# Kernel optimization log

Measured on AMD Instinct MI355X. Metric: run time of the kernel, lower is better.

The kernel has to match this reference:

```python
import jax, jax.numpy as jnp
import numpy as np

B, S, D, H, F, M = 2, 2048, 1024, 16, 4096, 1024
HD = D // H
LR, MOM_DECAY, WD, THRESH = 0.01, 0.9, 0.01, 0.1


def rmsnorm(x, w, eps=1e-8):
    n = jnp.linalg.norm(x, axis=-1, keepdims=True) * (x.shape[-1] ** -0.5)
    return w * x / (n + eps)


def rope_sin_cos(seq_len, dim):
    inv_freq = 1.0 / (10000.0 ** (jnp.arange(0, dim, 2, dtype=jnp.float32) / dim))
    ang = jnp.arange(seq_len, dtype=jnp.float32)[:, None] * inv_freq[None, :]  # [S, dim/2]
    return jnp.sin(ang), jnp.cos(ang)


def apply_rope(x, sin, cos):
    # x: [B,H,S,hd]; sin/cos: [S,hd/2] broadcast. Matches torch source:
    # split even/odd lanes, then CONCATENATE halves (not interleave).
    x1, x2 = x[..., ::2], x[..., 1::2]
    return jnp.concatenate([x1 * cos - x2 * sin, x1 * sin + x2 * cos], axis=-1)


def lmm_mlp(z, w0, b0, w1, b1):
    return jnp.maximum(z @ w0 + b0, 0.0) @ w1 + b1


def setup_inputs() -> dict:
    key = jax.random.key(0)
    k = jax.random.split(key, 20)
    sc = 0.02
    r = lambda i, shape: jax.random.normal(k[i], shape, jnp.float32) * sc
    return {
        'x': jax.random.normal(k[0], (B, S, D), jnp.float32),
        'mask': jnp.tril(jnp.ones((1, 1, S, S), dtype=bool)),
        'wq': r(1, (D, D)), 'wk': r(2, (D, D)), 'wv': r(3, (D, D)), 'wo': r(4, (D, D)),
        'n1': jnp.ones(D, jnp.float32), 'n2': jnp.ones(D, jnp.float32), 'n3': jnp.ones(D, jnp.float32),
        'ffn_w1': r(5, (D, F)), 'ffn_w2': r(6, (D, F)), 'ffn_w3': r(7, (F, D)),
        'pk_w': r(8, (D, M)), 'pk_b': jnp.zeros(M, jnp.float32),
        'pv_w': r(9, (D, M)), 'pv_b': jnp.zeros(M, jnp.float32),
        'pq_w': r(10, (D, M)), 'pq_b': jnp.zeros(M, jnp.float32),
        'l0_w': r(11, (M, M)), 'l0_b': jnp.zeros(M, jnp.float32),
        'l1_w': r(12, (M, M)), 'l1_b': jnp.zeros(M, jnp.float32),
        'm0_w': jnp.zeros((M, M), jnp.float32), 'm0_b': jnp.zeros(M, jnp.float32),
        'm1_w': jnp.zeros((M, M), jnp.float32), 'm1_b': jnp.zeros(M, jnp.float32),
    }


def reference(x, mask, wq, wk, wv, wo, n1, n2, n3, ffn_w1, ffn_w2, ffn_w3,
              pk_w, pk_b, pv_w, pv_b, pq_w, pq_b,
              l0_w, l0_b, l1_w, l1_b, m0_w, m0_b, m1_w, m1_b):
    # ---- attention sublayer (pre-norm, RoPE) ----
    hn = rmsnorm(x, n1)
    q = (hn @ wq).reshape(B, S, H, HD).transpose(0, 2, 1, 3)
    kk = (hn @ wk).reshape(B, S, H, HD).transpose(0, 2, 1, 3)
    v = (hn @ wv).reshape(B, S, H, HD).transpose(0, 2, 1, 3)
    sin, cos = rope_sin_cos(S, HD)
    q = apply_rope(q, sin, cos)
    kk = apply_rope(kk, sin, cos)
    scores = jnp.einsum('bhqd,bhkd->bhqk', q, kk) / np.sqrt(HD).astype(np.float32)
    scores = jnp.where(mask, scores, -jnp.inf)
    attn = jax.nn.softmax(scores, axis=-1)
    o = jnp.einsum('bhqk,bhkd->bhqd', attn, v).transpose(0, 2, 1, 3).reshape(B, S, D)
    h = x + o @ wo

    # ---- neural memory sublayer ----
    hn2 = rmsnorm(h, n2)
    q_lmm = hn2 @ pq_w + pq_b
    retrieved = lmm_mlp(q_lmm, l0_w, l0_b, l1_w, l1_b)  # uses PRE-update params

    # online Titan-style LMM update (torch does this under no_grad, after retrieval)
    kf = jax.lax.stop_gradient((hn2 @ pk_w + pk_b).reshape(B * S, M))
    vf = jax.lax.stop_gradient((hn2 @ pv_w + pv_b).reshape(B * S, M))

    def lmm_loss(params):
        pred = lmm_mlp(kf, *params)
        return jnp.sum(jnp.mean((pred - vf) ** 2, axis=-1))

    params = (l0_w, l0_b, l1_w, l1_b)
    loss_sum, grads = jax.value_and_grad(lmm_loss)(params)
    avg_loss = loss_sum / (B * S)
    do_update = avg_loss >= THRESH
    moms = (m0_w, m0_b, m1_w, m1_b)
    new_moms, new_params = [], []
    for p, m, g in zip(params, moms, grads):
        nm = MOM_DECAY * m - LR * g
        np_ = p * (1.0 - WD) + nm
        new_moms.append(jnp.where(do_update, nm, m))
        new_params.append(jnp.where(do_update, np_, p))

    h = h + retrieved

    # ---- SwiGLU FFN sublayer ----
    hn3 = rmsnorm(h, n3)
    ffn = (jax.nn.silu(hn3 @ ffn_w1) * (hn3 @ ffn_w2)) @ ffn_w3
    out = h + ffn
    return (out, *new_params, *new_moms)
```

## Files before the change

### kernel.cpp

```cpp
#include <hip/hip_runtime.h>
#include <cstdint>
#include <cstddef>

typedef __bf16 bf16;
typedef __bf16 bf16x2 __attribute__((ext_vector_type(2)));
typedef __bf16 bf16x4 __attribute__((ext_vector_type(4)));
typedef __bf16 bf16x8 __attribute__((ext_vector_type(8)));
typedef float  f32x4  __attribute__((ext_vector_type(4)));
typedef __attribute__((address_space(1))) unsigned int u32_g;
typedef __attribute__((address_space(3))) unsigned int u32_l;

#define DI __device__ __forceinline__

constexpr int Bc = 2, Sc = 2048, Dc = 1024, Hc = 16, HDc = 64, Fc = 4096, Mc = 1024;
constexpr int NTc = Bc * Sc;

DI void llds16(const bf16* g, bf16* l) {
  __builtin_amdgcn_global_load_lds((const u32_g*)g, (u32_l*)l, 16, 0, 0);
}
DI f32x4 cvt4(bf16x4 a) {
  f32x4 r; r[0] = (float)a[0]; r[1] = (float)a[1]; r[2] = (float)a[2]; r[3] = (float)a[3];
  return r;
}

__global__ void k_detect(const unsigned short* __restrict__ x, int* __restrict__ flag)
{
  const int tid = threadIdx.x;
  int cnt = 0;
#pragma unroll
  for (int i = 0; i < 8; i++) {
    unsigned short h = x[tid * 8 + i];
    int e = (h >> 7) & 0xFF;
    if (e < 96 || e > 160) cnt++;
  }
#pragma unroll
  for (int off = 32; off > 0; off >>= 1) cnt += __shfl_down(cnt, off, 64);
  if (tid == 0) *flag = (cnt > 32) ? 1 : 0;
}

__global__ __launch_bounds__(256)
void k_cvt(const void* __restrict__ src, bf16* __restrict__ dst, int n4, const int* __restrict__ flag)
{
  int i = blockIdx.x * 256 + threadIdx.x;
  if (i >= n4) return;
  bf16x4 o;
  if (*flag) {
    f32x4 v = ((const f32x4*)src)[i];
    o[0] = (bf16)v[0]; o[1] = (bf16)v[1]; o[2] = (bf16)v[2]; o[3] = (bf16)v[3];
  } else {
    o = ((const bf16x4*)src)[i];
  }
  ((bf16x4*)dst)[i] = o;
}

__global__ void k_transpose_dt(const void* __restrict__ src, bf16* __restrict__ dst,
                               int R, int C, const int* __restrict__ flag)
{
  __shared__ bf16 tile[32][33];
  const int c0 = blockIdx.x * 32, r0 = blockIdx.y * 32;
  const int tx = threadIdx.x, ty = threadIdx.y;
  const bool f32 = (*flag != 0);
  for (int i = ty; i < 32; i += 8) {
    size_t idx = (size_t)(r0 + i) * C + (c0 + tx);
    tile[i][tx] = f32 ? (bf16)((const float*)src)[idx] : ((const bf16*)src)[idx];
  }
  __syncthreads();
  for (int i = ty; i < 32; i += 8)
    dst[(size_t)(c0 + i) * R + (r0 + tx)] = tile[tx][i];
}

__global__ void k_transpose_v(const bf16* __restrict__ v, bf16* __restrict__ vt)
{
  __shared__ bf16 tile[32][33];
  const int d0 = blockIdx.x * 32, s0 = blockIdx.y * 32;
  const int bh = blockIdx.z;
  const int b = bh >> 4, hh = bh & 15;
  const int tx = threadIdx.x, ty = threadIdx.y;
  for (int i = ty; i < 32; i += 8)
    tile[i][tx] = v[((size_t)(b * Sc + s0 + i)) * Dc + hh * HDc + d0 + tx];
  __syncthreads();
  for (int i = ty; i < 32; i += 8)
    vt[((size_t)(bh * HDc + d0 + i)) * Sc + s0 + tx] = tile[tx][i];
}

enum EpiMode { EPI_BF16 = 0, EPI_BIAS_BF16, EPI_BIAS_RELU_BF16, EPI_BIAS_RESB_F32,
               EPI_SILU_BF16, EPI_DZ_BF16, EPI_RESX_BF16, EPI_RESF_F32 };

template <int EPI>
__global__ __launch_bounds__(256)
void k_gemm(const bf16* __restrict__ A, const bf16* __restrict__ Bt,
            int Mr, int Nr, int Kr,
            float* outF, bf16* outB,
            const bf16* __restrict__ bias, const bf16* auxB,
            const float* resF,
            const void* __restrict__ resX, const int* __restrict__ flag)
{
  __shared__ bf16 As[128 * 32];
  __shared__ bf16 Bs[128 * 32];
  const int tid = threadIdx.x;
  const int w = tid >> 6, l = tid & 63;
  const int wr = w >> 1, wc = w & 1;
  const int row0 = blockIdx.y * 128, col0 = blockIdx.x * 128;

  const f32x4 vzero = {0.f, 0.f, 0.f, 0.f};
  f32x4 acc[4][4];
#pragma unroll
  for (int i = 0; i < 4; i++)
#pragma unroll
    for (int j = 0; j < 4; j++) acc[i][j] = vzero;

  const bf16* Ag = A + (size_t)(row0 + w * 16 + (l >> 2)) * Kr + ((l & 3) << 3);
  const bf16* Bg = Bt + (size_t)(col0 + w * 16 + (l >> 2)) * Kr + ((l & 3) << 3);
  bf16* AsW = &As[w * 512];
  bf16* BsW = &Bs[w * 512];
  const size_t rowHop = (size_t)64 * Kr;

  for (int k0 = 0; k0 < Kr; k0 += 32) {
    __syncthreads();
    llds16(Ag + k0, AsW);
    llds16(Ag + rowHop + k0, AsW + 2048);
    llds16(Bg + k0, BsW);
    llds16(Bg + rowHop + k0, BsW + 2048);
    __syncthreads();
    bf16x8 af[4], bfr[4];
#pragma unroll
    for (int mt = 0; mt < 4; mt++)
      af[mt] = *(const bf16x8*)&As[(wr * 64 + mt * 16 + (l & 15)) * 32 + (l >> 4) * 8];
#pragma unroll
    for (int nt = 0; nt < 4; nt++)
      bfr[nt] = *(const bf16x8*)&Bs[(wc * 64 + nt * 16 + (l & 15)) * 32 + (l >> 4) * 8];
#pragma unroll
    for (int mt = 0; mt < 4; mt++)
#pragma unroll
      for (int nt = 0; nt < 4; nt++)
        acc[mt][nt] = __builtin_amdgcn_mfma_f32_16x16x32_bf16(af[mt], bfr[nt], acc[mt][nt], 0, 0, 0);
  }

  const bool f32res = (EPI == EPI_RESX_BF16) ? (*flag != 0) : false;
  float biasv[4];
  if (EPI == EPI_BIAS_BF16 || EPI == EPI_BIAS_RELU_BF16 || EPI == EPI_BIAS_RESB_F32) {
#pragma unroll
    for (int nt = 0; nt < 4; nt++)
      biasv[nt] = (float)bias[col0 + wc * 64 + nt * 16 + (l & 15)];
  }
#pragma unroll
  for (int mt = 0; mt < 4; mt++) {
    const int rowb = row0 + wr * 64 + mt * 16 + ((l >> 4) << 2);
    float av[4][4];
    if (EPI == EPI_SILU_BF16 || EPI == EPI_DZ_BF16 || EPI == EPI_BIAS_RESB_F32) {
#pragma unroll
      for (int nt = 0; nt < 4; nt++) {
        const int col = col0 + wc * 64 + nt * 16 + (l & 15);
#pragma unroll
        for (int r = 0; r < 4; r++)
          av[nt][r] = (float)auxB[(size_t)(rowb + r) * Nr + col];
      }
    }
    if (EPI == EPI_RESF_F32) {
#pragma unroll
      for (int nt = 0; nt < 4; nt++) {
        const int col = col0 + wc * 64 + nt * 16 + (l & 15);
#pragma unroll
        for (int r = 0; r < 4; r++)
          av[nt][r] = resF[(size_t)(rowb + r) * Nr + col];
      }
    }
    if (EPI == EPI_RESX_BF16) {
#pragma unroll
      for (int nt = 0; nt < 4; nt++) {
        const int col = col0 + wc * 64 + nt * 16 + (l & 15);
#pragma unroll
        for (int r = 0; r < 4; r++) {
          const size_t idx = (size_t)(rowb + r) * Nr + col;
          av[nt][r] = f32res ? ((const float*)resX)[idx] : (float)((const bf16*)resX)[idx];
        }
      }
    }
#pragma unroll
    for (int nt = 0; nt < 4; nt++) {
      const int col = col0 + wc * 64 + nt * 16 + (l & 15);
#pragma unroll
      for (int r = 0; r < 4; r++) {
        const size_t idx = (size_t)(rowb + r) * Nr + col;
        float v = acc[mt][nt][r];
        if (EPI == EPI_BF16) { outB[idx] = (bf16)v; }
        else if (EPI == EPI_BIAS_BF16) { outB[idx] = (bf16)(v + biasv[nt]); }
        else if (EPI == EPI_BIAS_RELU_BF16) { outB[idx] = (bf16)fmaxf(v + biasv[nt], 0.f); }
        else if (EPI == EPI_BIAS_RESB_F32) { outF[idx] = v + biasv[nt] + av[nt][r]; }
        else if (EPI == EPI_SILU_BF16) {
          float s1v = av[nt][r];
          float sl = s1v / (1.f + __expf(-s1v));
          outB[idx] = (bf16)(sl * v);
        }
        else if (EPI == EPI_DZ_BF16) { outB[idx] = (bf16)(av[nt][r] > 0.f ? v : 0.f); }
        else if (EPI == EPI_RESX_BF16) { outB[idx] = (bf16)(v + av[nt][r]); }
        else if (EPI == EPI_RESF_F32) { outF[idx] = v + av[nt][r]; }
      }
    }
  }
}

__global__ __launch_bounds__(256)
void k_gemm_tn(const bf16* __restrict__ X, const bf16* __restrict__ Y, int Kt,
               float* __restrict__ out)
{
  __shared__ bf16 As[128 * 36];
  __shared__ bf16 Bs[128 * 36];
  const int tid = threadIdx.x;
  const int w = tid >> 6, l = tid & 63;
  const int wr = w >> 1, wc = w & 1;
  const int row0 = blockIdx.y * 128, col0 = blockIdx.x * 128;
  const int iofs = (tid & 15) * 8;
  const int tp   = (tid >> 4) * 2;

  const f32x4 vzero = {0.f, 0.f, 0.f, 0.f};
  f32x4 acc[4][4];
#pragma unroll
  for (int i = 0; i < 4; i++)
#pragma unroll
    for (int j = 0; j < 4; j++) acc[i][j] = vzero;

  const int chunk = Kt / gridDim.z;
  const int tbeg = blockIdx.z * chunk;

  for (int t0 = tbeg; t0 < tbeg + chunk; t0 += 32) {
    __syncthreads();
    bf16x8 a0 = *(const bf16x8*)&X[(size_t)(t0 + tp) * 1024 + row0 + iofs];
    bf16x8 a1 = *(const bf16x8*)&X[(size_t)(t0 + tp + 1) * 1024 + row0 + iofs];
    bf16x8 b0 = *(const bf16x8*)&Y[(size_t)(t0 + tp) * 1024 + col0 + iofs];
    bf16x8 b1 = *(const bf16x8*)&Y[(size_t)(t0 + tp + 1) * 1024 + col0 + iofs];
#pragma unroll
    for (int e = 0; e < 8; e++) {
      bf16x2 pa; pa[0] = a0[e]; pa[1] = a1[e];
      bf16x2 pb; pb[0] = b0[e]; pb[1] = b1[e];
      *(bf16x2*)&As[(iofs + e) * 36 + tp] = pa;
      *(bf16x2*)&Bs[(iofs + e) * 36 + tp] = pb;
    }
    __syncthreads();
    bf16x8 af[4], bfr[4];
#pragma unroll
    for (int mt = 0; mt < 4; mt++) {
      const int base = (wr * 64 + mt * 16 + (l & 15)) * 36 + (l >> 4) * 8;
      bf16x4 lo = *(const bf16x4*)&As[base];
      bf16x4 hi = *(const bf16x4*)&As[base + 4];
#pragma unroll
      for (int e = 0; e < 4; e++) { af[mt][e] = lo[e]; af[mt][4 + e] = hi[e]; }
    }
#pragma unroll
    for (int nt = 0; nt < 4; nt++) {
      const int base = (wc * 64 + nt * 16 + (l & 15)) * 36 + (l >> 4) * 8;
      bf16x4 lo = *(const bf16x4*)&Bs[base];
      bf16x4 hi = *(const bf16x4*)&Bs[base + 4];
#pragma unroll
      for (int e = 0; e < 4; e++) { bfr[nt][e] = lo[e]; bfr[nt][4 + e] = hi[e]; }
    }
#pragma unroll
    for (int mt = 0; mt < 4; mt++)
#pragma unroll
      for (int nt = 0; nt < 4; nt++)
        acc[mt][nt] = __builtin_amdgcn_mfma_f32_16x16x32_bf16(af[mt], bfr[nt], acc[mt][nt], 0, 0, 0);
  }

#pragma unroll
  for (int mt = 0; mt < 4; mt++) {
    const int rowb = row0 + wr * 64 + mt * 16 + ((l >> 4) << 2);
#pragma unroll
    for (int nt = 0; nt < 4; nt++) {
      const int col = col0 + wc * 64 + nt * 16 + (l & 15);
#pragma unroll
      for (int r = 0; r < 4; r++)
        atomicAdd(&out[(size_t)(rowb + r) * 1024 + col], acc[mt][nt][r]);
    }
  }
}

__global__ __launch_bounds__(256)
void k_rmsnorm_dt(const void* __restrict__ x, const bf16* __restrict__ w, bf16* __restrict__ out,
                  const int* __restrict__ flag)
{
  const int row = blockIdx.x;
  const int tid = threadIdx.x;
  f32x4 xv;
  if (*flag) xv = *(const f32x4*)((const float*)x + (size_t)row * Dc + tid * 4);
  else       xv = cvt4(*(const bf16x4*)((const bf16*)x + (size_t)row * Dc + tid * 4));
  float ss = xv[0] * xv[0] + xv[1] * xv[1] + xv[2] * xv[2] + xv[3] * xv[3];
#pragma unroll
  for (int off = 32; off > 0; off >>= 1) ss += __shfl_down(ss, off, 64);
  __shared__ float part[4];
  if ((tid & 63) == 0) part[tid >> 6] = ss;
  __syncthreads();
  float tot = part[0] + part[1] + part[2] + part[3];
  float inv = 1.f / (sqrtf(tot) * 0.03125f + 1e-8f);
  bf16x4 wb = *(const bf16x4*)(w + tid * 4);
  bf16x4 ov;
  ov[0] = (bf16)((float)wb[0] * xv[0] * inv);
  ov[1] = (bf16)((float)wb[1] * xv[1] * inv);
  ov[2] = (bf16)((float)wb[2] * xv[2] * inv);
  ov[3] = (bf16)((float)wb[3] * xv[3] * inv);
  *(bf16x4*)(out + (size_t)row * Dc + tid * 4) = ov;
}

__global__ __launch_bounds__(256)
void k_rmsnorm_b(const bf16* __restrict__ x, const bf16* __restrict__ w, bf16* __restrict__ out)
{
  const int row = blockIdx.x;
  const int tid = threadIdx.x;
  f32x4 xv = cvt4(*(const bf16x4*)(x + (size_t)row * Dc + tid * 4));
  float ss = xv[0] * xv[0] + xv[1] * xv[1] + xv[2] * xv[2] + xv[3] * xv[3];
#pragma unroll
  for (int off = 32; off > 0; off >>= 1) ss += __shfl_down(ss, off, 64);
  __shared__ float part[4];
  if ((tid & 63) == 0) part[tid >> 6] = ss;
  __syncthreads();
  float tot = part[0] + part[1] + part[2] + part[3];
  float inv = 1.f / (sqrtf(tot) * 0.03125f + 1e-8f);
  bf16x4 wb = *(const bf16x4*)(w + tid * 4);
  bf16x4 ov;
  ov[0] = (bf16)((float)wb[0] * xv[0] * inv);
  ov[1] = (bf16)((float)wb[1] * xv[1] * inv);
  ov[2] = (bf16)((float)wb[2] * xv[2] * inv);
  ov[3] = (bf16)((float)wb[3] * xv[3] * inv);
  *(bf16x4*)(out + (size_t)row * Dc + tid * 4) = ov;
}

__global__ __launch_bounds__(256)
void k_rmsnorm_f(const float* __restrict__ x, const bf16* __restrict__ w, bf16* __restrict__ out)
{
  const int row = blockIdx.x;
  const int tid = threadIdx.x;
  f32x4 xv = *(const f32x4*)(x + (size_t)row * Dc + tid * 4);
  float ss = xv[0] * xv[0] + xv[1] * xv[1] + xv[2] * xv[2] + xv[3] * xv[3];
#pragma unroll
  for (int off = 32; off > 0; off >>= 1) ss += __shfl_down(ss, off, 64);
  __shared__ float part[4];
  if ((tid & 63) == 0) part[tid >> 6] = ss;
  __syncthreads();
  float tot = part[0] + part[1] + part[2] + part[3];
  float inv = 1.f / (sqrtf(tot) * 0.03125f + 1e-8f);
  bf16x4 wb = *(const bf16x4*)(w + tid * 4);
  bf16x4 ov;
  ov[0] = (bf16)((float)wb[0] * xv[0] * inv);
  ov[1] = (bf16)((float)wb[1] * xv[1] * inv);
  ov[2] = (bf16)((float)wb[2] * xv[2] * inv);
  ov[3] = (bf16)((float)wb[3] * xv[3] * inv);
  *(bf16x4*)(out + (size_t)row * Dc + tid * 4) = ov;
}

__global__ __launch_bounds__(256)
void k_rope(bf16* __restrict__ q, bf16* __restrict__ kx)
{
  const int idx = blockIdx.x * 256 + threadIdx.x;
  const int t = idx >> 4, hh = idx & 15;
  const int s = t & (Sc - 1);
  float sn[32], cs[32];
#pragma unroll
  for (int i = 0; i < 32; i++) {
    float f = expf(-(float)i * 0.28782313662425574f);
    float ang = (float)s * f;
    sn[i] = sinf(ang);
    cs[i] = cosf(ang);
  }
  for (int pass = 0; pass < 2; pass++) {
    bf16* p = (pass ? kx : q) + (size_t)t * Dc + hh * HDc;
    float xb[64], ob[64];
#pragma unroll
    for (int j = 0; j < 16; j++) *(f32x4*)&xb[j * 4] = cvt4(*(const bf16x4*)(p + j * 4));
#pragma unroll
    for (int i = 0; i < 32; i++) {
      float x1 = xb[2 * i], x2 = xb[2 * i + 1];
      ob[i] = x1 * cs[i] - x2 * sn[i];
      ob[32 + i] = x1 * sn[i] + x2 * cs[i];
    }
#pragma unroll
    for (int j = 0; j < 16; j++) {
      bf16x4 o4;
      o4[0] = (bf16)ob[j * 4]; o4[1] = (bf16)ob[j * 4 + 1];
      o4[2] = (bf16)ob[j * 4 + 2]; o4[3] = (bf16)ob[j * 4 + 3];
      *(bf16x4*)(p + j * 4) = o4;
    }
  }
}

__global__ __launch_bounds__(256)
void k_attn(const bf16* __restrict__ q, const bf16* __restrict__ kx,
            const bf16* __restrict__ vt, bf16* __restrict__ o)
{
  constexpr int PAD = 72;
  __shared__ __align__(16) char smem[19456];

  const int blk = blockIdx.x;
  const int qi = 127 - (blk >> 5);
  const int bh = blk & 31;
  const int b = bh >> 4, hh = bh & 15;
  const int tid = threadIdx.x;
  const int w = tid >> 6, l = tid & 63;
  const int quad = l >> 4, c = l & 15;

  bf16* Psw = (bf16*)smem + w * 16 * PAD;
  float* Buf = (float*)smem;

  const int qrow = qi * 16 + c;
  const size_t qbase = ((size_t)(b * Sc + qrow)) * Dc + hh * HDc;
  bf16x8 qf0 = *(const bf16x8*)(q + qbase + quad * 8);
  bf16x8 qf1 = *(const bf16x8*)(q + qbase + 32 + quad * 8);
#pragma unroll
  for (int j = 0; j < 8; j++) {
    qf0[j] = (bf16)((float)qf0[j] * 0.125f);
    qf1[j] = (bf16)((float)qf1[j] * 0.125f);
  }

  const f32x4 vzero = {0.f, 0.f, 0.f, 0.f};
  f32x4 oacc[4];
#pragma unroll
  for (int nt = 0; nt < 4; nt++) oacc[nt] = vzero;
  float mrun[4] = {-3.0e38f, -3.0e38f, -3.0e38f, -3.0e38f};
  float lrun[4] = {0.f, 0.f, 0.f, 0.f};

  const int qrow0 = qi * 16 + quad * 4;
  const int ntiles = (qi >> 2) + 1;

  const bf16* kb = kx + (size_t)b * Sc * Dc + hh * HDc;
  const bf16* vb = vt + (size_t)bh * HDc * Sc;

  for (int t0 = w; t0 < ntiles; t0 += 4) {
    const int kk0 = t0 * 64;

    f32x4 sf[4];
#pragma unroll
    for (int nt = 0; nt < 4; nt++) {
      const bf16* kr = kb + (size_t)(kk0 + nt * 16 + c) * Dc + quad * 8;
      bf16x8 k0 = *(const bf16x8*)kr;
      bf16x8 k1 = *(const bf16x8*)(kr + 32);
      f32x4 a = vzero;
      a = __builtin_amdgcn_mfma_f32_16x16x32_bf16(qf0, k0, a, 0, 0, 0);
      a = __builtin_amdgcn_mfma_f32_16x16x32_bf16(qf1, k1, a, 0, 0, 0);
      sf[nt] = a;
    }
    if (t0 == ntiles - 1) {
#pragma unroll
      for (int nt = 0; nt < 4; nt++)
#pragma unroll
        for (int r = 0; r < 4; r++)
          if (kk0 + nt * 16 + c > qrow0 + r) sf[nt][r] = -3.0e38f;
    }

    float mnew[4], alpha[4];
#pragma unroll
    for (int r = 0; r < 4; r++) {
      float mt = fmaxf(fmaxf(sf[0][r], sf[1][r]), fmaxf(sf[2][r], sf[3][r]));
      mt = fmaxf(mt, __shfl_xor(mt, 1, 64));
      mt = fmaxf(mt, __shfl_xor(mt, 2, 64));
      mt = fmaxf(mt, __shfl_xor(mt, 4, 64));
      mt = fmaxf(mt, __shfl_xor(mt, 8, 64));
      mnew[r] = fmaxf(mrun[r], mt);
      alpha[r] = __expf(mrun[r] - mnew[r]);
      mrun[r] = mnew[r];
    }
    float ps[4] = {0.f, 0.f, 0.f, 0.f};
#pragma unroll
    for (int nt = 0; nt < 4; nt++)
#pragma unroll
      for (int r = 0; r < 4; r++) {
        float p = __expf(sf[nt][r] - mnew[r]);
        sf[nt][r] = p;
        ps[r] += p;
      }
#pragma unroll
    for (int r = 0; r < 4; r++) {
      ps[r] += __shfl_xor(ps[r], 1, 64);
      ps[r] += __shfl_xor(ps[r], 2, 64);
      ps[r] += __shfl_xor(ps[r], 4, 64);
      ps[r] += __shfl_xor(ps[r], 8, 64);
      lrun[r] = lrun[r] * alpha[r] + ps[r];
    }
#pragma unroll
    for (int nt = 0; nt < 4; nt++)
#pragma unroll
      for (int r = 0; r < 4; r++) oacc[nt][r] *= alpha[r];

#pragma unroll
    for (int nt = 0; nt < 4; nt++)
#pragma unroll
      for (int r = 0; r < 4; r++)
        Psw[(quad * 4 + r) * PAD + nt * 16 + c] = (bf16)sf[nt][r];
    bf16x8 pa0 = *(const bf16x8*)&Psw[c * PAD + quad * 8];
    bf16x8 pa1 = *(const bf16x8*)&Psw[c * PAD + 32 + quad * 8];

#pragma unroll
    for (int nt = 0; nt < 4; nt++) {
      const bf16* vr = vb + (size_t)(nt * 16 + c) * Sc + kk0 + quad * 8;
      bf16x8 v0 = *(const bf16x8*)vr;
      bf16x8 v1 = *(const bf16x8*)(vr + 32);
      oacc[nt] = __builtin_amdgcn_mfma_f32_16x16x32_bf16(pa0, v0, oacc[nt], 0, 0, 0);
      oacc[nt] = __builtin_amdgcn_mfma_f32_16x16x32_bf16(pa1, v1, oacc[nt], 0, 0, 0);
    }
  }

  __syncthreads();
  if (w > 0) {
    float* dst = Buf + ((w - 1) * 64 + l) * 25;
#pragma unroll
    for (int nt = 0; nt < 4; nt++)
#pragma unroll
      for (int r = 0; r < 4; r++) dst[nt * 4 + r] = oacc[nt][r];
#pragma unroll
    for (int r = 0; r < 4; r++) { dst[16 + r] = mrun[r]; dst[20 + r] = lrun[r]; }
  }
  __syncthreads();
  if (w == 0) {
#pragma unroll
    for (int w2 = 0; w2 < 3; w2++) {
      const float* src = Buf + (w2 * 64 + l) * 25;
      float m2[4], l2[4];
#pragma unroll
      for (int r = 0; r < 4; r++) { m2[r] = src[16 + r]; l2[r] = src[20 + r]; }
#pragma unroll
      for (int r = 0; r < 4; r++) {
        float mn = fmaxf(mrun[r], m2[r]);
        float a = __expf(mrun[r] - mn);
        float bb = __expf(m2[r] - mn);
        lrun[r] = lrun[r] * a + l2[r] * bb;
        mrun[r] = mn;
#pragma unroll
        for (int nt = 0; nt < 4; nt++)
          oacc[nt][r] = oacc[nt][r] * a + src[nt * 4 + r] * bb;
      }
    }
    float inv[4];
#pragma unroll
    for (int r = 0; r < 4; r++) inv[r] = 1.f / lrun[r];
#pragma unroll
    for (int r = 0; r < 4; r++) {
      const size_t obase = ((size_t)(b * Sc + qrow0 + r)) * Dc + hh * HDc;
#pragma unroll
      for (int nt = 0; nt < 4; nt++)
        o[obase + nt * 16 + c] = (bf16)(oacc[nt][r] * inv[r]);
    }
  }
}

__global__ __launch_bounds__(256)
void k_relu(const bf16* __restrict__ src, bf16* __restrict__ dst)
{
  int i = blockIdx.x * 256 + threadIdx.x;
  bf16x8 v = ((const bf16x8*)src)[i];
  bf16x8 o;
#pragma unroll
  for (int e = 0; e < 8; e++) o[e] = ((float)v[e] > 0.f) ? v[e] : (bf16)0.f;
  ((bf16x8*)dst)[i] = o;
}

__global__ __launch_bounds__(256)
void k_dpred(bf16* __restrict__ predDp, const bf16* __restrict__ vf, float* __restrict__ loss)
{
  __shared__ float red[4];
  const int tid = threadIdx.x;
  const size_t n8 = (size_t)NTc * Mc / 8;
  float lacc = 0.f;
  for (size_t i = (size_t)blockIdx.x * 256 + tid; i < n8; i += (size_t)gridDim.x * 256) {
    bf16x8 p8 = ((const bf16x8*)predDp)[i];
    bf16x8 v8 = ((const bf16x8*)vf)[i];
    bf16x8 d8;
#pragma unroll
    for (int e = 0; e < 8; e++) {
      float df = (float)p8[e] - (float)v8[e];
      lacc += df * df;
      d8[e] = (bf16)(df * (2.0f / 1024.0f));
    }
    ((bf16x8*)predDp)[i] = d8;
  }
#pragma unroll
  for (int off = 32; off > 0; off >>= 1) lacc += __shfl_down(lacc, off, 64);
  if ((tid & 63) == 0) red[tid >> 6] = lacc;
  __syncthreads();
  if (tid == 0) atomicAdd(loss, red[0] + red[1] + red[2] + red[3]);
}

__global__ __launch_bounds__(256)
void k_colsum(const bf16* __restrict__ X, float* __restrict__ out, int C, int rowsPer)
{
  int c = blockIdx.x * 256 + threadIdx.x;
  int r0 = blockIdx.y * rowsPer;
  float s = 0.f;
#pragma unroll 8
  for (int r = r0; r < r0 + rowsPer; r++) s += (float)X[(size_t)r * C + c];
  atomicAdd(&out[c], s);
}

__global__ __launch_bounds__(256)
void k_update_dt(const void* __restrict__ p0w, const void* __restrict__ p0b,
                 const void* __restrict__ p1w, const void* __restrict__ p1b,
                 const void* __restrict__ m0w, const void* __restrict__ m0b,
                 const void* __restrict__ m1w, const void* __restrict__ m1b,
                 const float* __restrict__ g0wF, const float* __restrict__ g0b,
                 const float* __restrict__ g1wF, const float* __restrict__ g1b,
                 const float* __restrict__ loss, const int* __restrict__ flag,
                 float* __restrict__ outP, float* __restrict__ outM)
{
  const int i = blockIdx.x * 256 + threadIdx.x;
  const bool upd = (loss[0] >= 0.1f * 1024.f * 4096.f);
  const bool f32 = (*flag != 0);
  constexpr int W = 1024 * 1024;
  const void *pp, *pm; int j; float g;
  if (i < W) { pp = p0w; pm = m0w; j = i; g = g0wF[i]; }
  else if (i < W + 1024) { j = i - W; pp = p0b; pm = m0b; g = g0b[j]; }
  else if (i < 2 * W + 1024) { j = i - W - 1024; pp = p1w; pm = m1w; g = g1wF[j]; }
  else { j = i - 2 * W - 1024; pp = p1b; pm = m1b; g = g1b[j]; }
  float p = f32 ? ((const float*)pp)[j] : (float)((const bf16*)pp)[j];
  float m = f32 ? ((const float*)pm)[j] : (float)((const bf16*)pm)[j];
  float nm = 0.9f * m - 0.01f * g;
  float np = 0.99f * p + nm;
  outP[i] = upd ? np : p;
  outM[i] = upd ? nm : m;
}

extern "C" void kernel_launch(void* const* d_in, const int* in_sizes, int n_in,
                              void* d_out, int out_size, void* d_ws, size_t ws_size,
                              hipStream_t stream)
{
  (void)in_sizes; (void)n_in; (void)out_size; (void)ws_size;
  const void* x   = d_in[0];
  const void* wq  = d_in[2];
  const void* wk  = d_in[3];
  const void* wv  = d_in[4];
  const void* wo  = d_in[5];
  const void* n1  = d_in[6];
  const void* n2  = d_in[7];
  const void* n3  = d_in[8];
  const void* fw1 = d_in[9];
  const void* fw2 = d_in[10];
  const void* fw3 = d_in[11];
  const void* pkw = d_in[12];
  const void* pkb = d_in[13];
  const void* pvw = d_in[14];
  const void* pvb = d_in[15];
  const void* pqw = d_in[16];
  const void* pqb = d_in[17];
  const void* l0w = d_in[18];
  const void* l0b = d_in[19];
  const void* l1w = d_in[20];
  const void* l1b = d_in[21];
  const void* m0w = d_in[22];
  const void* m0b = d_in[23];
  const void* m1w = d_in[24];
  const void* m1b = d_in[25];

  char* ws = (char*)d_ws;
  size_t off = 0;
  auto alloc = [&](size_t bytes) -> char* {
    char* p = ws + off;
    off += (bytes + 255) & ~(size_t)255;
    return p;
  };

  const size_t DD = (size_t)Dc * Dc;
  const size_t ND = (size_t)NTc * Dc;
  const size_t MB8 = 2 * ND;
  const size_t M1 = DD;

  bf16* W = (bf16*)alloc(2 * 8 * M1);
  bf16 *wqT = W, *wkT = W + M1, *wvT = W + 2 * M1, *woT = W + 3 * M1;
  bf16 *pqT = W + 4 * M1, *pkT = W + 5 * M1, *pvT = W + 6 * M1, *l0T = W + 7 * M1;
  bf16 *l1T = W + M1;
  bf16 *l1c = W;
  bf16 *w1T = W + 4 * M1;
  bf16 *w2T = W;
  bf16 *w3T = W + 4 * M1;

  bf16* B0 = (bf16*)alloc(MB8);
  bf16* B1 = (bf16*)alloc(MB8);
  bf16* B2 = (bf16*)alloc(MB8);
  bf16* B3 = (bf16*)alloc(MB8);
  bf16* B4 = (bf16*)alloc(MB8);
  bf16* s1 = B0;
  bf16* VtG = B4;

  float* g0b = (float*)alloc(4 * 1024);
  float* g1b = (float*)alloc(4 * 1024);
  float* lossb = (float*)alloc(256);
  int*   flag  = (int*)alloc(256);
  bf16* n1c = (bf16*)alloc(2 * 1024);
  bf16* n2c = (bf16*)alloc(2 * 1024);
  bf16* n3c = (bf16*)alloc(2 * 1024);
  bf16* bqc = (bf16*)alloc(2 * 1024);
  bf16* bkc = (bf16*)alloc(2 * 1024);
  bf16* bvc = (bf16*)alloc(2 * 1024);
  bf16* b0c = (bf16*)alloc(2 * 1024);
  bf16* b1c = (bf16*)alloc(2 * 1024);

  float* outX = (float*)d_out;
  float* outP = outX + ND;
  float* outM = outP + (2 * DD + 2048);
  float* g0wF = outM;
  float* g1wF = outM + M1 + 1024;
  bf16*  hn   = (bf16*)outX;

  const dim3 tb(32, 8);

  hipMemsetAsync(lossb, 0, sizeof(float), stream);
  hipMemsetAsync(g0b, 0, 4 * 1024, stream);
  hipMemsetAsync(g1b, 0, 4 * 1024, stream);
  hipMemsetAsync(outM, 0, (2 * M1 + 2048) * sizeof(float), stream);
  k_detect<<<1, 64, 0, stream>>>((const unsigned short*)x, flag);

  k_cvt<<<1, 256, 0, stream>>>(n1, n1c, 256, flag);
  k_cvt<<<1, 256, 0, stream>>>(n2, n2c, 256, flag);
  k_cvt<<<1, 256, 0, stream>>>(n3, n3c, 256, flag);
  k_cvt<<<1, 256, 0, stream>>>(pqb, bqc, 256, flag);
  k_cvt<<<1, 256, 0, stream>>>(pkb, bkc, 256, flag);
  k_cvt<<<1, 256, 0, stream>>>(pvb, bvc, 256, flag);
  k_cvt<<<1, 256, 0, stream>>>(l0b, b0c, 256, flag);
  k_cvt<<<1, 256, 0, stream>>>(l1b, b1c, 256, flag);

  k_transpose_dt<<<dim3(32, 32), tb, 0, stream>>>(wq, wqT, Dc, Dc, flag);
  k_transpose_dt<<<dim3(32, 32), tb, 0, stream>>>(wk, wkT, Dc, Dc, flag);
  k_transpose_dt<<<dim3(32, 32), tb, 0, stream>>>(wv, wvT, Dc, Dc, flag);
  k_transpose_dt<<<dim3(32, 32), tb, 0, stream>>>(wo, woT, Dc, Dc, flag);
  k_transpose_dt<<<dim3(32, 32), tb, 0, stream>>>(pqw, pqT, Dc, Mc, flag);
  k_transpose_dt<<<dim3(32, 32), tb, 0, stream>>>(pkw, pkT, Dc, Mc, flag);
  k_transpose_dt<<<dim3(32, 32), tb, 0, stream>>>(pvw, pvT, Dc, Mc, flag);
  k_transpose_dt<<<dim3(32, 32), tb, 0, stream>>>(l0w, l0T, Mc, Mc, flag);

  k_rmsnorm_dt<<<NTc, 256, 0, stream>>>(x, n1c, hn, flag);
  k_gemm<EPI_BF16><<<dim3(8, 32), 256, 0, stream>>>(hn, wqT, NTc, Dc, Dc, nullptr, B0, nullptr, nullptr, nullptr, nullptr, nullptr);
  k_gemm<EPI_BF16><<<dim3(8, 32), 256, 0, stream>>>(hn, wkT, NTc, Dc, Dc, nullptr, B1, nullptr, nullptr, nullptr, nullptr, nullptr);
  k_gemm<EPI_BF16><<<dim3(8, 32), 256, 0, stream>>>(hn, wvT, NTc, Dc, Dc, nullptr, B2, nullptr, nullptr, nullptr, nullptr, nullptr);
  k_transpose_v<<<dim3(2, 64, 32), tb, 0, stream>>>(B2, VtG);
  k_rope<<<256, 256, 0, stream>>>(B0, B1);
  k_attn<<<4096, 256, 0, stream>>>(B0, B1, VtG, B3);
  k_gemm<EPI_RESX_BF16><<<dim3(8, 32), 256, 0, stream>>>(B3, woT, NTc, Dc, Dc, nullptr, B4, nullptr, nullptr, nullptr, x, flag);
  k_transpose_dt<<<dim3(32, 32), tb, 0, stream>>>(l1w, l1T, Mc, Mc, flag);

  k_rmsnorm_b<<<NTc, 256, 0, stream>>>(B4, n2c, B0);
  k_gemm<EPI_BIAS_BF16><<<dim3(8, 32), 256, 0, stream>>>(B0, pqT, NTc, Mc, Dc, nullptr, B1, bqc, nullptr, nullptr, nullptr, nullptr);
  k_gemm<EPI_BIAS_BF16><<<dim3(8, 32), 256, 0, stream>>>(B0, pkT, NTc, Mc, Dc, nullptr, B2, bkc, nullptr, nullptr, nullptr, nullptr);
  k_gemm<EPI_BIAS_BF16><<<dim3(8, 32), 256, 0, stream>>>(B0, pvT, NTc, Mc, Dc, nullptr, B3, bvc, nullptr, nullptr, nullptr, nullptr);
  k_gemm<EPI_BIAS_RELU_BF16><<<dim3(8, 32), 256, 0, stream>>>(B1, l0T, NTc, Mc, Mc, nullptr, B0, b0c, nullptr, nullptr, nullptr, nullptr);
  k_gemm<EPI_BIAS_RESB_F32><<<dim3(8, 32), 256, 0, stream>>>(B0, l1T, NTc, Mc, Mc, outX, nullptr, b1c, B4, nullptr, nullptr, nullptr);

  k_gemm<EPI_BIAS_BF16><<<dim3(8, 32), 256, 0, stream>>>(B2, l0T, NTc, Mc, Mc, nullptr, B4, b0c, nullptr, nullptr, nullptr, nullptr);
  k_transpose_dt<<<dim3(128, 32), tb, 0, stream>>>(fw1, w1T, Dc, Fc, flag);
  k_relu<<<2048, 256, 0, stream>>>(B4, B0);
  k_gemm<EPI_BIAS_BF16><<<dim3(8, 32), 256, 0, stream>>>(B0, l1T, NTc, Mc, Mc, nullptr, B1, b1c, nullptr, nullptr, nullptr, nullptr);
  k_cvt<<<1024, 256, 0, stream>>>(l1w, l1c, (int)(DD / 4), flag);
  k_dpred<<<256, 256, 0, stream>>>(B1, B3, lossb);
  k_gemm<EPI_DZ_BF16><<<dim3(8, 32), 256, 0, stream>>>(B1, l1c, NTc, Mc, Mc, nullptr, B3, nullptr, B4, nullptr, nullptr, nullptr);
  k_gemm_tn<<<dim3(8, 8, 8), 256, 0, stream>>>(B0, B1, NTc, g1wF);
  k_gemm_tn<<<dim3(8, 8, 8), 256, 0, stream>>>(B2, B3, NTc, g0wF);
  k_colsum<<<dim3(4, 32), 256, 0, stream>>>(B1, g1b, Mc, NTc / 32);
  k_colsum<<<dim3(4, 32), 256, 0, stream>>>(B3, g0b, Mc, NTc / 32);
  k_update_dt<<<8200, 256, 0, stream>>>(l0w, l0b, l1w, l1b, m0w, m0b, m1w, m1b,
                                        g0wF, g0b, g1wF, g1b, lossb, flag, outP, outM);

  k_transpose_dt<<<dim3(128, 32), tb, 0, stream>>>(fw2, w2T, Dc, Fc, flag);
  k_rmsnorm_f<<<NTc, 256, 0, stream>>>(outX, n3c, B4);
  k_gemm<EPI_BF16><<<dim3(32, 32), 256, 0, stream>>>(B4, w1T, NTc, Fc, Dc, nullptr, s1, nullptr, nullptr, nullptr, nullptr, nullptr);
  k_transpose_dt<<<dim3(32, 128), tb, 0, stream>>>(fw3, w3T, Fc, Dc, flag);
  k_gemm<EPI_SILU_BF16><<<dim3(32, 32), 256, 0, stream>>>(B4, w2T, NTc, Fc, Dc, nullptr, s1, nullptr, s1, nullptr, nullptr, nullptr);
  k_gemm<EPI_RESF_F32><<<dim3(8, 32), 256, 0, stream>>>(s1, w3T, NTc, Dc, Fc, outX, nullptr, nullptr, nullptr, outX, nullptr, nullptr);
}
```

Before: 1.091 ms.

## Batch QKV and LMM projections into wide GEMMs, split-K final FFN with atomics

The three Q/K/V projections become one N=3072 GEMM, and the three LMM pq/pk/pv projections become another, each writing into separate output segments. The two l0 forward passes (retrieval and key path) are merged into one 2*NT-row GEMM with a fused ReLU, which drops the separate relu kernel and one GEMM launch. The final FFN down-projection is split along K into two slices that accumulate into the residual output with float atomicAdd, giving more blocks for this long-K GEMM. The changes assume the projection weight transposes and the B buffers sit contiguously in memory, and the atomic accumulation makes the floating-point summation order nondeterministic.

```diff
diff --git a/kernel.cpp b/kernel.cpp
--- a/kernel.cpp
+++ b/kernel.cpp
@@ -84,7 +84,8 @@
 }
 
 enum EpiMode { EPI_BF16 = 0, EPI_BIAS_BF16, EPI_BIAS_RELU_BF16, EPI_BIAS_RESB_F32,
-               EPI_SILU_BF16, EPI_DZ_BF16, EPI_RESX_BF16, EPI_RESF_F32 };
+               EPI_SILU_BF16, EPI_DZ_BF16, EPI_RESX_BF16, EPI_RESF_F32,
+               EPI_SEGC_BF16, EPI_SEGC_BIAS_BF16, EPI_SEG2_RELU_BF16, EPI_ATOMIC_F32 };
 
 template <int EPI>
 __global__ __launch_bounds__(256)
@@ -115,7 +116,10 @@
   bf16* BsW = &Bs[w * 512];
   const size_t rowHop = (size_t)64 * Kr;
 
-  for (int k0 = 0; k0 < Kr; k0 += 32) {
+  const int chunk = Kr / gridDim.z;
+  const int kbeg = blockIdx.z * chunk;
+
+  for (int k0 = kbeg; k0 < kbeg + chunk; k0 += 32) {
     __syncthreads();
     llds16(Ag + k0, AsW);
     llds16(Ag + rowHop + k0, AsW + 2048);
@@ -138,7 +142,8 @@
 
   const bool f32res = (EPI == EPI_RESX_BF16) ? (*flag != 0) : false;
   float biasv[4];
-  if (EPI == EPI_BIAS_BF16 || EPI == EPI_BIAS_RELU_BF16 || EPI == EPI_BIAS_RESB_F32) {
+  if (EPI == EPI_BIAS_BF16 || EPI == EPI_BIAS_RELU_BF16 || EPI == EPI_BIAS_RESB_F32 ||
+      EPI == EPI_SEGC_BIAS_BF16 || EPI == EPI_SEG2_RELU_BF16) {
 #pragma unroll
     for (int nt = 0; nt < 4; nt++)
       biasv[nt] = (float)bias[col0 + wc * 64 + nt * 16 + (l & 15)];
@@ -195,6 +200,19 @@
         else if (EPI == EPI_DZ_BF16) { outB[idx] = (bf16)(av[nt][r] > 0.f ? v : 0.f); }
         else if (EPI == EPI_RESX_BF16) { outB[idx] = (bf16)(v + av[nt][r]); }
         else if (EPI == EPI_RESF_F32) { outF[idx] = v + av[nt][r]; }
+        else if (EPI == EPI_SEGC_BF16 || EPI == EPI_SEGC_BIAS_BF16) {
+          const size_t sidx = (size_t)(col >> 10) * ((size_t)NTc * 1024)
+                            + (size_t)(rowb + r) * 1024 + (col & 1023);
+          float vv = (EPI == EPI_SEGC_BIAS_BF16) ? (v + biasv[nt]) : v;
+          outB[sidx] = (bf16)vv;
+        }
+        else if (EPI == EPI_SEG2_RELU_BF16) {
+          bf16* ob = (rowb >> 12) ? (bf16*)outF : outB;
+          ob[(size_t)((rowb + r) & 4095) * 1024 + col] = (bf16)fmaxf(v + biasv[nt], 0.f);
+        }
+        else if (EPI == EPI_ATOMIC_F32) {
+          atomicAdd(&outF[(size_t)(rowb + r) * Nr + col], v);
+        }
       }
     }
   }
@@ -537,17 +555,6 @@
         o[obase + nt * 16 + c] = (bf16)(oacc[nt][r] * inv[r]);
     }
   }
-}
-
-__global__ __launch_bounds__(256)
-void k_relu(const bf16* __restrict__ src, bf16* __restrict__ dst)
-{
-  int i = blockIdx.x * 256 + threadIdx.x;
-  bf16x8 v = ((const bf16x8*)src)[i];
-  bf16x8 o;
-#pragma unroll
-  for (int e = 0; e < 8; e++) o[e] = ((float)v[e] > 0.f) ? v[e] : (bf16)0.f;
-  ((bf16x8*)dst)[i] = o;
 }
 
 __global__ __launch_bounds__(256)
@@ -662,6 +669,7 @@
   bf16 *wqT = W, *wkT = W + M1, *wvT = W + 2 * M1, *woT = W + 3 * M1;
   bf16 *pqT = W + 4 * M1, *pkT = W + 5 * M1, *pvT = W + 6 * M1, *l0T = W + 7 * M1;
   bf16 *l1T = W + M1;
+  bf16 *h1buf = W + 2 * M1;
   bf16 *l1c = W;
   bf16 *w1T = W + 4 * M1;
   bf16 *w2T = W;
@@ -682,9 +690,7 @@
   bf16* n1c = (bf16*)alloc(2 * 1024);
   bf16* n2c = (bf16*)alloc(2 * 1024);
   bf16* n3c = (bf16*)alloc(2 * 1024);
-  bf16* bqc = (bf16*)alloc(2 * 1024);
-  bf16* bkc = (bf16*)alloc(2 * 1024);
-  bf16* bvc = (bf16*)alloc(2 * 1024);
+  bf16* bqkv = (bf16*)alloc(2 * 3072);
   bf16* b0c = (bf16*)alloc(2 * 1024);
   bf16* b1c = (bf16*)alloc(2 * 1024);
 
@@ -706,9 +712,9 @@
   k_cvt<<<1, 256, 0, stream>>>(n1, n1c, 256, flag);
   k_cvt<<<1, 256, 0, stream>>>(n2, n2c, 256, flag);
   k_cvt<<<1, 256, 0, stream>>>(n3, n3c, 256, flag);
-  k_cvt<<<1, 256, 0, stream>>>(pqb, bqc, 256, flag);
-  k_cvt<<<1, 256, 0, stream>>>(pkb, bkc, 256, flag);
-  k_cvt<<<1, 256, 0, stream>>>(pvb, bvc, 256, flag);
+  k_cvt<<<1, 256, 0, stream>>>(pqb, bqkv, 256, flag);
+  k_cvt<<<1, 256, 0, stream>>>(pkb, bqkv + 1024, 256, flag);
+  k_cvt<<<1, 256, 0, stream>>>(pvb, bqkv + 2048, 256, flag);
   k_cvt<<<1, 256, 0, stream>>>(l0b, b0c, 256, flag);
   k_cvt<<<1, 256, 0, stream>>>(l1b, b1c, 256, flag);
 
@@ -722,9 +728,7 @@
   k_transpose_dt<<<dim3(32, 32), tb, 0, stream>>>(l0w, l0T, Mc, Mc, flag);
 
   k_rmsnorm_dt<<<NTc, 256, 0, stream>>>(x, n1c, hn, flag);
-  k_gemm<EPI_BF16><<<dim3(8, 32), 256, 0, stream>>>(hn, wqT, NTc, Dc, Dc, nullptr, B0, nullptr, nullptr, nullptr, nullptr, nullptr);
-  k_gemm<EPI_BF16><<<dim3(8, 32), 256, 0, stream>>>(hn, wkT, NTc, Dc, Dc, nullptr, B1, nullptr, nullptr, nullptr, nullptr, nullptr);
-  k_gemm<EPI_BF16><<<dim3(8, 32), 256, 0, stream>>>(hn, wvT, NTc, Dc, Dc, nullptr, B2, nullptr, nullptr, nullptr, nullptr, nullptr);
+  k_gemm<EPI_SEGC_BF16><<<dim3(24, 32), 256, 0, stream>>>(hn, wqT, NTc, 3072, Dc, nullptr, B0, nullptr, nullptr, nullptr, nullptr, nullptr);
   k_transpose_v<<<dim3(2, 64, 32), tb, 0, stream>>>(B2, VtG);
   k_rope<<<256, 256, 0, stream>>>(B0, B1);
   k_attn<<<4096, 256, 0, stream>>>(B0, B1, VtG, B3);
@@ -732,21 +736,17 @@
   k_transpose_dt<<<dim3(32, 32), tb, 0, stream>>>(l1w, l1T, Mc, Mc, flag);
 
   k_rmsnorm_b<<<NTc, 256, 0, stream>>>(B4, n2c, B0);
-  k_gemm<EPI_BIAS_BF16><<<dim3(8, 32), 256, 0, stream>>>(B0, pqT, NTc, Mc, Dc, nullptr, B1, bqc, nullptr, nullptr, nullptr, nullptr);
-  k_gemm<EPI_BIAS_BF16><<<dim3(8, 32), 256, 0, stream>>>(B0, pkT, NTc, Mc, Dc, nullptr, B2, bkc, nullptr, nullptr, nullptr, nullptr);
-  k_gemm<EPI_BIAS_BF16><<<dim3(8, 32), 256, 0, stream>>>(B0, pvT, NTc, Mc, Dc, nullptr, B3, bvc, nullptr, nullptr, nullptr, nullptr);
-  k_gemm<EPI_BIAS_RELU_BF16><<<dim3(8, 32), 256, 0, stream>>>(B1, l0T, NTc, Mc, Mc, nullptr, B0, b0c, nullptr, nullptr, nullptr, nullptr);
+  k_gemm<EPI_SEGC_BIAS_BF16><<<dim3(24, 32), 256, 0, stream>>>(B0, pqT, NTc, 3072, Dc, nullptr, B1, bqkv, nullptr, nullptr, nullptr, nullptr);
+  k_gemm<EPI_SEG2_RELU_BF16><<<dim3(8, 64), 256, 0, stream>>>(B1, l0T, 2 * NTc, Mc, Mc, (float*)h1buf, B0, b0c, nullptr, nullptr, nullptr, nullptr);
   k_gemm<EPI_BIAS_RESB_F32><<<dim3(8, 32), 256, 0, stream>>>(B0, l1T, NTc, Mc, Mc, outX, nullptr, b1c, B4, nullptr, nullptr, nullptr);
-
-  k_gemm<EPI_BIAS_BF16><<<dim3(8, 32), 256, 0, stream>>>(B2, l0T, NTc, Mc, Mc, nullptr, B4, b0c, nullptr, nullptr, nullptr, nullptr);
-  k_transpose_dt<<<dim3(128, 32), tb, 0, stream>>>(fw1, w1T, Dc, Fc, flag);
-  k_relu<<<2048, 256, 0, stream>>>(B4, B0);
-  k_gemm<EPI_BIAS_BF16><<<dim3(8, 32), 256, 0, stream>>>(B0, l1T, NTc, Mc, Mc, nullptr, B1, b1c, nullptr, nullptr, nullptr, nullptr);
+  k_gemm<EPI_BIAS_BF16><<<dim3(8, 32), 256, 0, stream>>>(h1buf, l1T, NTc, Mc, Mc, nullptr, B1, b1c, nullptr, nullptr, nullptr, nullptr);
+
   k_cvt<<<1024, 256, 0, stream>>>(l1w, l1c, (int)(DD / 4), flag);
   k_dpred<<<256, 256, 0, stream>>>(B1, B3, lossb);
-  k_gemm<EPI_DZ_BF16><<<dim3(8, 32), 256, 0, stream>>>(B1, l1c, NTc, Mc, Mc, nullptr, B3, nullptr, B4, nullptr, nullptr, nullptr);
-  k_gemm_tn<<<dim3(8, 8, 8), 256, 0, stream>>>(B0, B1, NTc, g1wF);
+  k_gemm<EPI_DZ_BF16><<<dim3(8, 32), 256, 0, stream>>>(B1, l1c, NTc, Mc, Mc, nullptr, B3, nullptr, h1buf, nullptr, nullptr, nullptr);
+  k_gemm_tn<<<dim3(8, 8, 8), 256, 0, stream>>>(h1buf, B1, NTc, g1wF);
   k_gemm_tn<<<dim3(8, 8, 8), 256, 0, stream>>>(B2, B3, NTc, g0wF);
+  k_transpose_dt<<<dim3(128, 32), tb, 0, stream>>>(fw1, w1T, Dc, Fc, flag);
   k_colsum<<<dim3(4, 32), 256, 0, stream>>>(B1, g1b, Mc, NTc / 32);
   k_colsum<<<dim3(4, 32), 256, 0, stream>>>(B3, g0b, Mc, NTc / 32);
   k_update_dt<<<8200, 256, 0, stream>>>(l0w, l0b, l1w, l1b, m0w, m0b, m1w, m1b,
@@ -757,5 +757,5 @@
   k_gemm<EPI_BF16><<<dim3(32, 32), 256, 0, stream>>>(B4, w1T, NTc, Fc, Dc, nullptr, s1, nullptr, nullptr, nullptr, nullptr, nullptr);
   k_transpose_dt<<<dim3(32, 128), tb, 0, stream>>>(fw3, w3T, Fc, Dc, flag);
   k_gemm<EPI_SILU_BF16><<<dim3(32, 32), 256, 0, stream>>>(B4, w2T, NTc, Fc, Dc, nullptr, s1, nullptr, s1, nullptr, nullptr, nullptr);
-  k_gemm<EPI_RESF_F32><<<dim3(8, 32), 256, 0, stream>>>(s1, w3T, NTc, Dc, Fc, outX, nullptr, nullptr, nullptr, outX, nullptr, nullptr);
-}
+  k_gemm<EPI_ATOMIC_F32><<<dim3(8, 32, 2), 256, 0, stream>>>(s1, w3T, NTc, Dc, Fc, outX, nullptr, nullptr, nullptr, nullptr, nullptr, nullptr);
+}
```

New measurement: 980.7 us. 1.11x faster.
